# Optimization experiments

Measured on AMD Instinct MI355X. Metric: run time of the kernel, lower is better.

The kernel has to match this reference:

```python
import jax, jax.numpy as jnp
import numpy as np

TIN = 5
HDIM = 1024
N_HEADS = 16
HEAD_DIM = HDIM // N_HEADS
N_LAYERS = 8
FF_DIM = 4096
MAX_REL = 128
L_REL = 2 * MAX_REL + 1
NUM_CLASSES = 100
FEAT = 256
IN_DIM = TIN * FEAT
NEG = -1e9


def _ln(x, g, b, eps):
    m = jnp.mean(x, axis=-1, keepdims=True)
    v = jnp.mean(jnp.square(x - m), axis=-1, keepdims=True)
    return (x - m) * jax.lax.rsqrt(v + eps) * g + b


def setup_inputs() -> dict:
    key = jax.random.key(0)
    ks = jax.random.split(key, 16)
    s = 0.02
    inp = {
        'x': jax.random.normal(ks[0], (2, 5120, FEAT), dtype=jnp.float32),
        'pe_ln1_g': jnp.ones((IN_DIM,), jnp.float32),
        'pe_ln1_b': jnp.zeros((IN_DIM,), jnp.float32),
        'pe_w': jax.random.normal(ks[1], (HDIM, IN_DIM), jnp.float32) * s,
        'pe_b': jnp.zeros((HDIM,), jnp.float32),
        'pe_ln2_g': jnp.ones((HDIM,), jnp.float32),
        'pe_ln2_b': jnp.zeros((HDIM,), jnp.float32),
        'lnA_g': jnp.ones((N_LAYERS, HDIM), jnp.float32),
        'lnA_b': jnp.zeros((N_LAYERS, HDIM), jnp.float32),
        'qkv_w': jax.random.normal(ks[2], (N_LAYERS, 3 * HDIM, HDIM), jnp.float32) * s,
        'qkv_b': jnp.zeros((N_LAYERS, 3 * HDIM), jnp.float32),
        'out_w': jax.random.normal(ks[3], (N_LAYERS, HDIM, HDIM), jnp.float32) * s,
        'out_b': jnp.zeros((N_LAYERS, HDIM), jnp.float32),
        'lnF_g': jnp.ones((N_LAYERS, HDIM), jnp.float32),
        'lnF_b': jnp.zeros((N_LAYERS, HDIM), jnp.float32),
        'fc1_w': jax.random.normal(ks[4], (N_LAYERS, FF_DIM, HDIM), jnp.float32) * s,
        'fc1_b': jnp.zeros((N_LAYERS, FF_DIM), jnp.float32),
        'fc2_w': jax.random.normal(ks[5], (N_LAYERS, HDIM, FF_DIM), jnp.float32) * s,
        'fc2_b': jnp.zeros((N_LAYERS, HDIM), jnp.float32),
        'rel_table': jax.random.normal(ks[6], (N_HEADS, L_REL), jnp.float32) * s,
        'final_g': jnp.ones((HDIM,), jnp.float32),
        'final_b': jnp.zeros((HDIM,), jnp.float32),
        'head_w': jax.random.normal(ks[7], (NUM_CLASSES, HDIM), jnp.float32) * s,
        'head_b': jnp.zeros((NUM_CLASSES,), jnp.float32),
    }
    return inp


def reference(x, pe_ln1_g, pe_ln1_b, pe_w, pe_b, pe_ln2_g, pe_ln2_b,
              lnA_g, lnA_b, qkv_w, qkv_b, out_w, out_b,
              lnF_g, lnF_b, fc1_w, fc1_b, fc2_w, fc2_b,
              rel_table, final_g, final_b, head_w, head_b):
    B, T, F = x.shape
    n_patch = T // TIN  # static
    # Patch embedding
    z = x[:, :n_patch * TIN, :].reshape(B, n_patch, TIN * F)
    z = _ln(z, pe_ln1_g, pe_ln1_b, 1e-6)
    z = z @ pe_w.T + pe_b
    z = _ln(z, pe_ln2_g, pe_ln2_b, 1e-6)
    S = n_patch
    # Relative-position bias (H, S, S) + causal mask (intended semantics)
    pos = jnp.arange(S)
    rel = pos[None, :] - pos[:, None]
    clipped = jnp.clip(rel, -MAX_REL, MAX_REL) + MAX_REL
    bias = rel_table[:, clipped]  # (H, S, S)
    causal = jnp.where(pos[None, :] > pos[:, None], NEG, 0.0).astype(z.dtype)
    bias = bias + causal[None, :, :]
    scale = 1.0 / np.sqrt(HEAD_DIM)
    for l in range(N_LAYERS):
        h = _ln(z, lnA_g[l], lnA_b[l], 1e-5)
        qkv = h @ qkv_w[l].T + qkv_b[l]  # (B, S, 3*H*d)
        q, k, v = jnp.split(qkv, 3, axis=-1)
        q = q.reshape(B, S, N_HEADS, HEAD_DIM).transpose(0, 2, 1, 3)
        k = k.reshape(B, S, N_HEADS, HEAD_DIM).transpose(0, 2, 1, 3)
        v = v.reshape(B, S, N_HEADS, HEAD_DIM).transpose(0, 2, 1, 3)
        scores = jnp.einsum('bhqd,bhkd->bhqk', q, k) * scale + bias[None]
        attn = jax.nn.softmax(scores, axis=-1)
        o = jnp.einsum('bhqk,bhkd->bhqd', attn, v)
        o = o.transpose(0, 2, 1, 3).reshape(B, S, HDIM)
        z = z + (o @ out_w[l].T + out_b[l])
        f = _ln(z, lnF_g[l], lnF_b[l], 1e-5)
        f = jax.nn.gelu(f @ fc1_w[l].T + fc1_b[l], approximate=False)
        z = z + (f @ fc2_w[l].T + fc2_b[l])
    z = _ln(z, final_g, final_b, 1e-5)
    logits = z @ head_w.T + head_b  # (B, S, num_classes)
    return logits
```

## Files before the change

### kernel.cpp

```cpp
#include <hip/hip_runtime.h>
#include <cstdint>
#include <cstddef>


#define AS1 __attribute__((address_space(1)))
#define AS3 __attribute__((address_space(3)))

typedef unsigned short u16;
typedef __bf16 bf16x8v __attribute__((ext_vector_type(8)));
typedef unsigned short u16x8 __attribute__((ext_vector_type(8)));
typedef unsigned short u16x4 __attribute__((ext_vector_type(4)));
typedef float f32x4 __attribute__((ext_vector_type(4)));

__device__ __forceinline__ u16 f2b(float f) {
  union { float f; unsigned u; } x; x.f = f;
  unsigned r = x.u + 0x7FFFu + ((x.u >> 16) & 1u);
  return (u16)(r >> 16);
}

__global__ __launch_bounds__(256) void k_convert(const float* __restrict__ src,
                                                 u16* __restrict__ dst, int n8) {
  int i = blockIdx.x * 256 + threadIdx.x;
  if (i >= n8) return;
  const float4* s4 = (const float4*)src;
  float4 a = s4[2 * i], b = s4[2 * i + 1];
  u16x8 r;
  r[0] = f2b(a.x); r[1] = f2b(a.y); r[2] = f2b(a.z); r[3] = f2b(a.w);
  r[4] = f2b(b.x); r[5] = f2b(b.y); r[6] = f2b(b.z); r[7] = f2b(b.w);
  *(u16x8*)(dst + (size_t)i * 8) = r;
}

__global__ __launch_bounds__(256) void k_ln(const float* __restrict__ in,
                                            const float* __restrict__ gw,
                                            const float* __restrict__ bw,
                                            float* outf, u16* outb,
                                            int C, float eps) {
  int row = blockIdx.x, tid = threadIdx.x;
  int nv = C >> 2;
  const float4* in4 = (const float4*)(in + (size_t)row * C);
  float4 c0 = {0, 0, 0, 0}, c1 = {0, 0, 0, 0};
  float s1 = 0.f, s2 = 0.f;
  int cnt = 0;
  for (int i = tid; i < nv; i += 256) {
    float4 t = in4[i];
    if (cnt == 0) c0 = t; else c1 = t;
    cnt++;
    s1 += t.x + t.y + t.z + t.w;
    s2 += t.x * t.x + t.y * t.y + t.z * t.z + t.w * t.w;
  }
  __shared__ float red[8];
  for (int m = 32; m >= 1; m >>= 1) { s1 += __shfl_down(s1, m); s2 += __shfl_down(s2, m); }
  int wave = tid >> 6, lane = tid & 63;
  if (lane == 0) { red[wave * 2] = s1; red[wave * 2 + 1] = s2; }
  __syncthreads();
  s1 = red[0] + red[2] + red[4] + red[6];
  s2 = red[1] + red[3] + red[5] + red[7];
  float invC = 1.f / (float)C;
  float mean = s1 * invC;
  float var = s2 * invC - mean * mean;
  float rstd = rsqrtf(var + eps);
  const float4* g4 = (const float4*)gw;
  const float4* b4 = (const float4*)bw;
  cnt = 0;
  for (int i = tid; i < nv; i += 256) {
    float4 t = (cnt == 0) ? c0 : c1; cnt++;
    float4 gg = g4[i], bb = b4[i];
    float4 y;
    y.x = (t.x - mean) * rstd * gg.x + bb.x;
    y.y = (t.y - mean) * rstd * gg.y + bb.y;
    y.z = (t.z - mean) * rstd * gg.z + bb.z;
    y.w = (t.w - mean) * rstd * gg.w + bb.w;
    if (outf) *(float4*)(outf + (size_t)row * C + 4 * i) = y;
    if (outb) {
      u16x4 o;
      o[0] = f2b(y.x); o[1] = f2b(y.y); o[2] = f2b(y.z); o[3] = f2b(y.w);
      *(u16x4*)(outb + (size_t)row * C + 4 * i) = o;
    }
  }
}

#define EPI_F32 0
#define EPI_QKV 1
#define EPI_RES 2
#define EPI_GELU 3

template <int EPI>
__global__ __launch_bounds__(256) void k_gemm(const u16* __restrict__ A,
                                              const u16* __restrict__ B,
                                              const float* __restrict__ bias,
                                              const float* resid,
                                              float* outf, u16* outb,
                                              int K, int Nout) {
  int tid = threadIdx.x, wave = tid >> 6, lane = tid & 63;
  int n0 = blockIdx.x * 128, m0 = blockIdx.y * 128;
  __shared__ u16 As[128 * 64];
  __shared__ u16 Bs[128 * 64];
  f32x4 acc[4][4] = {};
  int wm = (wave >> 1) * 64, wn = (wave & 1) * 64;
  int cl = lane & 15, grp = lane >> 4;

  for (int k0 = 0; k0 < K; k0 += 64) {
#pragma unroll
    for (int i = 0; i < 4; i++) {
      int o = ((i * 4 + wave) << 10) + lane * 16;
      int row = o >> 7, col = (o & 127) >> 1;
      const u16* ga = A + (size_t)(m0 + row) * K + k0 + col;
      __builtin_amdgcn_global_load_lds((const AS1 void*)ga,
                                       (AS3 void*)(As + ((i * 4 + wave) << 9)),
                                       16, 0, 0);
      int rb = n0 + row;
      if (rb > Nout - 1) rb = Nout - 1;
      const u16* gb = B + (size_t)rb * K + k0 + col;
      __builtin_amdgcn_global_load_lds((const AS1 void*)gb,
                                       (AS3 void*)(Bs + ((i * 4 + wave) << 9)),
                                       16, 0, 0);
    }
    __syncthreads();
    bf16x8v a[4][2], b[4][2];
#pragma unroll
    for (int mf = 0; mf < 4; mf++)
#pragma unroll
      for (int kc = 0; kc < 2; kc++)
        a[mf][kc] = *(const bf16x8v*)(As + (wm + mf * 16 + cl) * 64 + kc * 32 + (grp << 3));
#pragma unroll
    for (int nf = 0; nf < 4; nf++)
#pragma unroll
      for (int kc = 0; kc < 2; kc++)
        b[nf][kc] = *(const bf16x8v*)(Bs + (wn + nf * 16 + cl) * 64 + kc * 32 + (grp << 3));
#pragma unroll
    for (int kc = 0; kc < 2; kc++)
#pragma unroll
      for (int mf = 0; mf < 4; mf++)
#pragma unroll
        for (int nf = 0; nf < 4; nf++)
          acc[mf][nf] = __builtin_amdgcn_mfma_f32_16x16x32_bf16(
              a[mf][kc], b[nf][kc], acc[mf][nf], 0, 0, 0);
    __syncthreads();
  }

#pragma unroll
  for (int nf = 0; nf < 4; nf++) {
    int gn = n0 + wn + nf * 16 + cl;
    bool nok = gn < Nout;
    float bv = nok ? bias[gn] : 0.f;
#pragma unroll
    for (int mf = 0; mf < 4; mf++)
#pragma unroll
      for (int r = 0; r < 4; r++) {
        int gm = m0 + wm + mf * 16 + grp * 4 + r;
        float v = acc[mf][nf][r] + bv;
        size_t oi = (size_t)gm * Nout + gn;
        if (EPI == EPI_F32) {
          if (nok) outf[oi] = v;
        } else if (EPI == EPI_RES) {
          if (nok) outf[oi] = resid[oi] + v;
        } else if (EPI == EPI_QKV) {
          if (gn < 1024) v *= 0.125f;
          if (nok) outb[oi] = f2b(v);
        } else {
          float gv = 0.5f * v * (1.f + erff(v * 0.70710678118654752f));
          if (nok) outb[oi] = f2b(gv);
        }
      }
  }
}

#define LSTR 72
__global__ __launch_bounds__(256) void k_attn(const u16* __restrict__ qkv,
                                              const float* __restrict__ rel_table,
                                              u16* __restrict__ obuf) {
  int tid = threadIdx.x, wave = tid >> 6, lane = tid & 63;
  int qt = blockIdx.x, bh = blockIdx.y;
  int bb = bh >> 4, h = bh & 15;
  __shared__ u16 Qs[64 * LSTR], Ks[64 * LSTR], Vs[64 * LSTR];
  __shared__ u16 Ps[4][16 * LSTR];
  __shared__ float rels[257];
  for (int i = tid; i < 257; i += 256) rels[i] = rel_table[h * 257 + i];
  int tokb = bb * 1024, qb = qt * 64;
  {
    int r = tid >> 2, c0 = (tid & 3) * 16;
    const u16* src = qkv + (size_t)(tokb + qb + r) * 3072 + h * 64 + c0;
    *(u16x8*)&Qs[r * LSTR + c0] = *(const u16x8*)src;
    *(u16x8*)&Qs[r * LSTR + c0 + 8] = *(const u16x8*)(src + 8);
  }
  __syncthreads();
  int cl = lane & 15, grp = lane >> 4;
  bf16x8v aq[2];
#pragma unroll
  for (int kc = 0; kc < 2; kc++)
    aq[kc] = *(const bf16x8v*)&Qs[(wave * 16 + cl) * LSTR + kc * 32 + (grp << 3)];
  f32x4 oacc[4] = {};
  float mrun[4] = {-1e30f, -1e30f, -1e30f, -1e30f};
  float lrun[4] = {0.f, 0.f, 0.f, 0.f};

  for (int kt = 0; kt <= qt; kt++) {
    {
      int r = tid >> 2, c0 = (tid & 3) * 16;
      const u16* ks = qkv + (size_t)(tokb + kt * 64 + r) * 3072 + 1024 + h * 64 + c0;
      *(u16x8*)&Ks[r * LSTR + c0] = *(const u16x8*)ks;
      *(u16x8*)&Ks[r * LSTR + c0 + 8] = *(const u16x8*)(ks + 8);
      const u16* vs = qkv + (size_t)(tokb + kt * 64 + r) * 3072 + 2048 + h * 64 + c0;
      u16x8 v0 = *(const u16x8*)vs, v1 = *(const u16x8*)(vs + 8);
#pragma unroll
      for (int j = 0; j < 8; j++) {
        Vs[(c0 + j) * LSTR + r] = v0[j];
        Vs[(c0 + 8 + j) * LSTR + r] = v1[j];
      }
    }
    __syncthreads();
    f32x4 sc[4] = {};
#pragma unroll
    for (int nf = 0; nf < 4; nf++)
#pragma unroll
      for (int kc = 0; kc < 2; kc++) {
        bf16x8v bk = *(const bf16x8v*)&Ks[(nf * 16 + cl) * LSTR + kc * 32 + (grp << 3)];
        sc[nf] = __builtin_amdgcn_mfma_f32_16x16x32_bf16(aq[kc], bk, sc[nf], 0, 0, 0);
      }
#pragma unroll
    for (int nf = 0; nf < 4; nf++) {
      int gk = kt * 64 + nf * 16 + cl;
#pragma unroll
      for (int r = 0; r < 4; r++) {
        int gq = qb + wave * 16 + grp * 4 + r;
        int d = gk - gq;
        int ci = (d < -128 ? -128 : (d > 128 ? 128 : d)) + 128;
        float bv = rels[ci];
        if (gk > gq) bv -= 1e9f;
        sc[nf][r] += bv;
      }
    }
    float ps[4][4];
#pragma unroll
    for (int r = 0; r < 4; r++) {
      float rmax = fmaxf(fmaxf(sc[0][r], sc[1][r]), fmaxf(sc[2][r], sc[3][r]));
      rmax = fmaxf(rmax, __shfl_xor(rmax, 1));
      rmax = fmaxf(rmax, __shfl_xor(rmax, 2));
      rmax = fmaxf(rmax, __shfl_xor(rmax, 4));
      rmax = fmaxf(rmax, __shfl_xor(rmax, 8));
      float mnew = fmaxf(mrun[r], rmax);
      float alpha = __expf(mrun[r] - mnew);
      float psum = 0.f;
#pragma unroll
      for (int nf = 0; nf < 4; nf++) {
        float p = __expf(sc[nf][r] - mnew);
        ps[nf][r] = p;
        psum += p;
      }
      psum += __shfl_xor(psum, 1);
      psum += __shfl_xor(psum, 2);
      psum += __shfl_xor(psum, 4);
      psum += __shfl_xor(psum, 8);
      lrun[r] = lrun[r] * alpha + psum;
      mrun[r] = mnew;
#pragma unroll
      for (int nf = 0; nf < 4; nf++) oacc[nf][r] *= alpha;
    }
#pragma unroll
    for (int nf = 0; nf < 4; nf++)
#pragma unroll
      for (int r = 0; r < 4; r++)
        Ps[wave][(grp * 4 + r) * LSTR + nf * 16 + cl] = f2b(ps[nf][r]);
    __syncthreads();
    bf16x8v ap[2];
#pragma unroll
    for (int kc = 0; kc < 2; kc++)
      ap[kc] = *(const bf16x8v*)&Ps[wave][cl * LSTR + kc * 32 + (grp << 3)];
#pragma unroll
    for (int nf = 0; nf < 4; nf++)
#pragma unroll
      for (int kc = 0; kc < 2; kc++) {
        bf16x8v bv = *(const bf16x8v*)&Vs[(nf * 16 + cl) * LSTR + kc * 32 + (grp << 3)];
        oacc[nf] = __builtin_amdgcn_mfma_f32_16x16x32_bf16(ap[kc], bv, oacc[nf], 0, 0, 0);
      }
    __syncthreads();
  }
#pragma unroll
  for (int r = 0; r < 4; r++) {
    float inv = 1.f / lrun[r];
    int gq = qb + wave * 16 + grp * 4 + r;
#pragma unroll
    for (int nf = 0; nf < 4; nf++)
      obuf[(size_t)(tokb + gq) * 1024 + h * 64 + nf * 16 + cl] = f2b(oacc[nf][r] * inv);
  }
}

extern "C" void kernel_launch(void* const* d_in, const int* in_sizes, int n_in,
                              void* d_out, int out_size, void* d_ws, size_t ws_size,
                              hipStream_t stream) {
  (void)in_sizes; (void)n_in; (void)out_size; (void)ws_size;
  const float* x        = (const float*)d_in[0];
  const float* pe_ln1_g = (const float*)d_in[1];
  const float* pe_ln1_b = (const float*)d_in[2];
  const float* pe_w     = (const float*)d_in[3];
  const float* pe_b     = (const float*)d_in[4];
  const float* pe_ln2_g = (const float*)d_in[5];
  const float* pe_ln2_b = (const float*)d_in[6];
  const float* lnA_g    = (const float*)d_in[7];
  const float* lnA_b    = (const float*)d_in[8];
  const float* qkv_w    = (const float*)d_in[9];
  const float* qkv_b    = (const float*)d_in[10];
  const float* out_w    = (const float*)d_in[11];
  const float* out_b    = (const float*)d_in[12];
  const float* lnF_g    = (const float*)d_in[13];
  const float* lnF_b    = (const float*)d_in[14];
  const float* fc1_w    = (const float*)d_in[15];
  const float* fc1_b    = (const float*)d_in[16];
  const float* fc2_w    = (const float*)d_in[17];
  const float* fc2_b    = (const float*)d_in[18];
  const float* rel      = (const float*)d_in[19];
  const float* fin_g    = (const float*)d_in[20];
  const float* fin_b    = (const float*)d_in[21];
  const float* head_w   = (const float*)d_in[22];
  const float* head_b   = (const float*)d_in[23];
  float* out = (float*)d_out;

  char* ws = (char*)d_ws;
  u16*   a_pe = (u16*)(ws);
  float* z    = (float*)(ws + 5242880);
  float* zpre = (float*)(ws + 13631488);
  u16*   hbuf = (u16*)(ws + 22020096);
  u16*   qkvb = (u16*)(ws + 26214400);
  u16*   ob   = (u16*)(ws + 38797312);
  u16*   fbuf = (u16*)(ws + 42991616);
  u16*   wbuf = (u16*)(ws + 59768832);

  auto conv = [&](const float* s, int n) {
    k_convert<<<dim3((n / 8 + 255) / 256), dim3(256), 0, stream>>>(s, wbuf, n / 8);
  };

  conv(pe_w, 1280 * 1024);
  k_ln<<<2048, 256, 0, stream>>>(x, pe_ln1_g, pe_ln1_b, nullptr, a_pe, 1280, 1e-6f);
  k_gemm<EPI_F32><<<dim3(8, 16), 256, 0, stream>>>(a_pe, wbuf, pe_b, nullptr, zpre, nullptr, 1280, 1024);
  k_ln<<<2048, 256, 0, stream>>>(zpre, pe_ln2_g, pe_ln2_b, z, nullptr, 1024, 1e-6f);

  for (int l = 0; l < 8; l++) {
    k_ln<<<2048, 256, 0, stream>>>(z, lnA_g + l * 1024, lnA_b + l * 1024, nullptr, hbuf, 1024, 1e-5f);
    conv(qkv_w + (size_t)l * 3145728, 3145728);
    k_gemm<EPI_QKV><<<dim3(24, 16), 256, 0, stream>>>(hbuf, wbuf, qkv_b + l * 3072, nullptr, nullptr, qkvb, 1024, 3072);
    k_attn<<<dim3(16, 32), 256, 0, stream>>>(qkvb, rel, ob);
    conv(out_w + (size_t)l * 1048576, 1048576);
    k_gemm<EPI_RES><<<dim3(8, 16), 256, 0, stream>>>(ob, wbuf, out_b + l * 1024, z, z, nullptr, 1024, 1024);
    k_ln<<<2048, 256, 0, stream>>>(z, lnF_g + l * 1024, lnF_b + l * 1024, nullptr, hbuf, 1024, 1e-5f);
    conv(fc1_w + (size_t)l * 4194304, 4194304);
    k_gemm<EPI_GELU><<<dim3(32, 16), 256, 0, stream>>>(hbuf, wbuf, fc1_b + l * 4096, nullptr, nullptr, fbuf, 1024, 4096);
    conv(fc2_w + (size_t)l * 4194304, 4194304);
    k_gemm<EPI_RES><<<dim3(8, 16), 256, 0, stream>>>(fbuf, wbuf, fc2_b + l * 1024, z, z, nullptr, 4096, 1024);
  }

  k_ln<<<2048, 256, 0, stream>>>(z, fin_g, fin_b, nullptr, hbuf, 1024, 1e-5f);
  conv(head_w, 102400);
  k_gemm<EPI_F32><<<dim3(1, 16), 256, 0, stream>>>(hbuf, wbuf, head_b, nullptr, out, nullptr, 1024, 100);
}
```

Measured before the change: 2.575 ms.

## Split-K the narrow GEMMs with atomic accumulation and batch weight conversions

```diff
diff --git a/kernel.cpp b/kernel.cpp
--- a/kernel.cpp
+++ b/kernel.cpp
@@ -28,6 +28,31 @@
   r[0] = f2b(a.x); r[1] = f2b(a.y); r[2] = f2b(a.z); r[3] = f2b(a.w);
   r[4] = f2b(b.x); r[5] = f2b(b.y); r[6] = f2b(b.z); r[7] = f2b(b.w);
   *(u16x8*)(dst + (size_t)i * 8) = r;
+}
+
+__global__ __launch_bounds__(256) void k_convert2(const float* __restrict__ s0,
+                                                  u16* __restrict__ d0, int n8_0,
+                                                  const float* __restrict__ s1,
+                                                  u16* __restrict__ d1, int n8_1) {
+  int i = blockIdx.x * 256 + threadIdx.x;
+  const float* s; u16* d; int j;
+  if (i < n8_0) { s = s0; d = d0; j = i; }
+  else { j = i - n8_0; if (j >= n8_1) return; s = s1; d = d1; }
+  const float4* s4 = (const float4*)s;
+  float4 a = s4[2 * j], b = s4[2 * j + 1];
+  u16x8 r;
+  r[0] = f2b(a.x); r[1] = f2b(a.y); r[2] = f2b(a.z); r[3] = f2b(a.w);
+  r[4] = f2b(b.x); r[5] = f2b(b.y); r[6] = f2b(b.z); r[7] = f2b(b.w);
+  *(u16x8*)(d + (size_t)j * 8) = r;
+}
+
+__global__ __launch_bounds__(256) void k_bias_init(float* __restrict__ out,
+                                                   const float* __restrict__ bias,
+                                                   int N, int total4) {
+  int i = blockIdx.x * 256 + threadIdx.x;
+  if (i >= total4) return;
+  int n = (i * 4) % N;
+  *(float4*)(out + (size_t)i * 4) = *(const float4*)(bias + n);
 }
 
 __global__ __launch_bounds__(256) void k_ln(const float* __restrict__ in,
@@ -79,38 +104,37 @@
   }
 }
 
-#define EPI_F32 0
 #define EPI_QKV 1
-#define EPI_RES 2
 #define EPI_GELU 3
+#define EPI_ATOM 4
 
 template <int EPI>
 __global__ __launch_bounds__(256) void k_gemm(const u16* __restrict__ A,
                                               const u16* __restrict__ B,
                                               const float* __restrict__ bias,
-                                              const float* resid,
                                               float* outf, u16* outb,
-                                              int K, int Nout) {
+                                              int Kstride, int Kc, int Nout) {
   int tid = threadIdx.x, wave = tid >> 6, lane = tid & 63;
   int n0 = blockIdx.x * 128, m0 = blockIdx.y * 128;
+  int kbeg = blockIdx.z * Kc, kend = kbeg + Kc;
   __shared__ u16 As[128 * 64];
   __shared__ u16 Bs[128 * 64];
   f32x4 acc[4][4] = {};
   int wm = (wave >> 1) * 64, wn = (wave & 1) * 64;
   int cl = lane & 15, grp = lane >> 4;
 
-  for (int k0 = 0; k0 < K; k0 += 64) {
+  for (int k0 = kbeg; k0 < kend; k0 += 64) {
 #pragma unroll
     for (int i = 0; i < 4; i++) {
       int o = ((i * 4 + wave) << 10) + lane * 16;
       int row = o >> 7, col = (o & 127) >> 1;
-      const u16* ga = A + (size_t)(m0 + row) * K + k0 + col;
+      const u16* ga = A + (size_t)(m0 + row) * Kstride + k0 + col;
       __builtin_amdgcn_global_load_lds((const AS1 void*)ga,
                                        (AS3 void*)(As + ((i * 4 + wave) << 9)),
                                        16, 0, 0);
       int rb = n0 + row;
       if (rb > Nout - 1) rb = Nout - 1;
-      const u16* gb = B + (size_t)rb * K + k0 + col;
+      const u16* gb = B + (size_t)rb * Kstride + k0 + col;
       __builtin_amdgcn_global_load_lds((const AS1 void*)gb,
                                        (AS3 void*)(Bs + ((i * 4 + wave) << 9)),
                                        16, 0, 0);
@@ -138,11 +162,12 @@
     __syncthreads();
   }
 
+  bool addb = (EPI != EPI_ATOM) || (blockIdx.z == 0 && bias != nullptr);
 #pragma unroll
   for (int nf = 0; nf < 4; nf++) {
     int gn = n0 + wn + nf * 16 + cl;
     bool nok = gn < Nout;
-    float bv = nok ? bias[gn] : 0.f;
+    float bv = (nok && addb) ? bias[gn] : 0.f;
 #pragma unroll
     for (int mf = 0; mf < 4; mf++)
 #pragma unroll
@@ -150,10 +175,8 @@
         int gm = m0 + wm + mf * 16 + grp * 4 + r;
         float v = acc[mf][nf][r] + bv;
         size_t oi = (size_t)gm * Nout + gn;
-        if (EPI == EPI_F32) {
-          if (nok) outf[oi] = v;
-        } else if (EPI == EPI_RES) {
-          if (nok) outf[oi] = resid[oi] + v;
+        if (EPI == EPI_ATOM) {
+          if (nok) unsafeAtomicAdd(&outf[oi], v);
         } else if (EPI == EPI_QKV) {
           if (gn < 1024) v *= 0.125f;
           if (nok) outb[oi] = f2b(v);
@@ -315,39 +338,41 @@
   float* out = (float*)d_out;
 
   char* ws = (char*)d_ws;
+  u16*   fbuf = (u16*)(ws);
   u16*   a_pe = (u16*)(ws);
-  float* z    = (float*)(ws + 5242880);
-  float* zpre = (float*)(ws + 13631488);
-  u16*   hbuf = (u16*)(ws + 22020096);
-  u16*   qkvb = (u16*)(ws + 26214400);
-  u16*   ob   = (u16*)(ws + 38797312);
-  u16*   fbuf = (u16*)(ws + 42991616);
-  u16*   wbuf = (u16*)(ws + 59768832);
-
-  auto conv = [&](const float* s, int n) {
-    k_convert<<<dim3((n / 8 + 255) / 256), dim3(256), 0, stream>>>(s, wbuf, n / 8);
-  };
-
-  conv(pe_w, 1280 * 1024);
+  float* zpre = (float*)(ws + 5242880);
+  float* z    = (float*)(ws + 16777216);
+  u16*   hbuf = (u16*)(ws + 25165824);
+  u16*   qkvb = (u16*)(ws + 29360128);
+  u16*   ob   = (u16*)(ws + 41943040);
+  u16*   wsl  = (u16*)(ws + 46137344);
+
+  k_convert<<<dim3(640), dim3(256), 0, stream>>>(pe_w, wsl, 163840);
   k_ln<<<2048, 256, 0, stream>>>(x, pe_ln1_g, pe_ln1_b, nullptr, a_pe, 1280, 1e-6f);
-  k_gemm<EPI_F32><<<dim3(8, 16), 256, 0, stream>>>(a_pe, wbuf, pe_b, nullptr, zpre, nullptr, 1280, 1024);
+  k_bias_init<<<dim3(2048), dim3(256), 0, stream>>>(zpre, pe_b, 1024, 524288);
+  k_gemm<EPI_ATOM><<<dim3(8, 16, 4), 256, 0, stream>>>(a_pe, wsl, nullptr, zpre, nullptr, 1280, 320, 1024);
   k_ln<<<2048, 256, 0, stream>>>(zpre, pe_ln2_g, pe_ln2_b, z, nullptr, 1024, 1e-6f);
 
   for (int l = 0; l < 8; l++) {
+    u16* wq = wsl;
+    u16* wo = wsl + 3145728;
+    u16* w1 = wsl;
+    u16* w2 = wsl + 4194304;
     k_ln<<<2048, 256, 0, stream>>>(z, lnA_g + l * 1024, lnA_b + l * 1024, nullptr, hbuf, 1024, 1e-5f);
-    conv(qkv_w + (size_t)l * 3145728, 3145728);
-    k_gemm<EPI_QKV><<<dim3(24, 16), 256, 0, stream>>>(hbuf, wbuf, qkv_b + l * 3072, nullptr, nullptr, qkvb, 1024, 3072);
+    k_convert2<<<dim3(2048), dim3(256), 0, stream>>>(qkv_w + (size_t)l * 3145728, wq, 393216,
+                                                     out_w + (size_t)l * 1048576, wo, 131072);
+    k_gemm<EPI_QKV><<<dim3(24, 16, 1), 256, 0, stream>>>(hbuf, wq, qkv_b + l * 3072, nullptr, qkvb, 1024, 1024, 3072);
     k_attn<<<dim3(16, 32), 256, 0, stream>>>(qkvb, rel, ob);
-    conv(out_w + (size_t)l * 1048576, 1048576);
-    k_gemm<EPI_RES><<<dim3(8, 16), 256, 0, stream>>>(ob, wbuf, out_b + l * 1024, z, z, nullptr, 1024, 1024);
+    k_gemm<EPI_ATOM><<<dim3(8, 16, 4), 256, 0, stream>>>(ob, wo, out_b + l * 1024, z, nullptr, 1024, 256, 1024);
     k_ln<<<2048, 256, 0, stream>>>(z, lnF_g + l * 1024, lnF_b + l * 1024, nullptr, hbuf, 1024, 1e-5f);
-    conv(fc1_w + (size_t)l * 4194304, 4194304);
-    k_gemm<EPI_GELU><<<dim3(32, 16), 256, 0, stream>>>(hbuf, wbuf, fc1_b + l * 4096, nullptr, nullptr, fbuf, 1024, 4096);
-    conv(fc2_w + (size_t)l * 4194304, 4194304);
-    k_gemm<EPI_RES><<<dim3(8, 16), 256, 0, stream>>>(fbuf, wbuf, fc2_b + l * 1024, z, z, nullptr, 4096, 1024);
+    k_convert2<<<dim3(4096), dim3(256), 0, stream>>>(fc1_w + (size_t)l * 4194304, w1, 524288,
+                                                     fc2_w + (size_t)l * 4194304, w2, 524288);
+    k_gemm<EPI_GELU><<<dim3(32, 16, 1), 256, 0, stream>>>(hbuf, w1, fc1_b + l * 4096, nullptr, fbuf, 1024, 1024, 4096);
+    k_gemm<EPI_ATOM><<<dim3(8, 16, 4), 256, 0, stream>>>(fbuf, w2, fc2_b + l * 1024, z, nullptr, 4096, 1024, 1024);
   }
 
   k_ln<<<2048, 256, 0, stream>>>(z, fin_g, fin_b, nullptr, hbuf, 1024, 1e-5f);
-  conv(head_w, 102400);
-  k_gemm<EPI_F32><<<dim3(1, 16), 256, 0, stream>>>(hbuf, wbuf, head_b, nullptr, out, nullptr, 1024, 100);
-}
+  k_convert<<<dim3(50), dim3(256), 0, stream>>>(head_w, wsl, 12800);
+  k_bias_init<<<dim3(200), dim3(256), 0, stream>>>(out, head_b, 100, 51200);
+  k_gemm<EPI_ATOM><<<dim3(1, 16, 4), 256, 0, stream>>>(hbuf, wsl, nullptr, out, nullptr, 1024, 256, 100);
+}
```

After: 2.160 ms. 16.1% less time.
